# Optimization experiments

Measured on AMD Instinct MI355X. Metric: run time of the kernel, lower is better.

The kernel has to match this reference:

```python
import jax, jax.numpy as jnp
import numpy as np

TOPK = 2
NUM_EXPERTS = 8


def setup_inputs() -> dict:
    key = jax.random.key(0)
    k1, k2 = jax.random.split(key)
    T, H, E = 16384, 2048, NUM_EXPERTS
    x = jax.random.normal(k1, (T, H), dtype=jnp.float32)
    W = jax.random.normal(k2, (E, H), dtype=jnp.float32) * (1.0 / np.sqrt(H))
    return {"x": x, "W": W}


def reference(x, W):
    # gating: [T, H] @ [H, E] -> [T, E]
    logits = jnp.einsum("th,eh->te", x, W)
    # top-k expert selection (largest, sorted desc, matching torch.topk)
    top_logits, top_indices = jax.lax.top_k(logits, TOPK)
    # softmax over the k selected logits, computed in fp32 (torch: dtype=float32 then type_as)
    scores = jax.nn.softmax(top_logits.astype(jnp.float32), axis=-1).astype(logits.dtype)
    # histogram of expert assignments (torch.histc -> float counts)
    tokens_per_expert = jnp.bincount(top_indices.reshape(-1), length=NUM_EXPERTS).astype(jnp.float32)
    return scores, top_indices, tokens_per_expert
```

## Files before the change

kernel.cpp:

```cpp
#include <hip/hip_runtime.h>
#include <math.h>

#define HDIM 2048
#define NEXP 8
#define TB 4
#define WPB 4
#define TPB (TB * WPB)

__global__ void router_main(const float* __restrict__ x,
                            const float* __restrict__ W,
                            float* __restrict__ out_scores,
                            float* __restrict__ out_idx,
                            float* __restrict__ hist_global,
                            float* __restrict__ partial,
                            int T)
{
    __shared__ int cnt[NEXP];
    if (threadIdx.x < NEXP) cnt[threadIdx.x] = 0;
    __syncthreads();

    const int lane  = threadIdx.x & 63;
    const int wv    = threadIdx.x >> 6;
    const int gwave = blockIdx.x * WPB + wv;
    const int tok0  = gwave * TB;

    float acc[TB * NEXP];
#pragma unroll
    for (int i = 0; i < TB * NEXP; ++i) acc[i] = 0.f;

#pragma unroll
    for (int iter = 0; iter < HDIM / 256; ++iter) {
        const int h = iter * 256 + lane * 4;
        float4 w[NEXP];
#pragma unroll
        for (int e = 0; e < NEXP; ++e)
            w[e] = *reinterpret_cast<const float4*>(W + e * HDIM + h);
#pragma unroll
        for (int t = 0; t < TB; ++t) {
            const int tt = min(tok0 + t, T - 1);
            float4 xv = *reinterpret_cast<const float4*>(x + (size_t)tt * HDIM + h);
#pragma unroll
            for (int e = 0; e < NEXP; ++e) {
                float a = acc[t * NEXP + e];
                a = fmaf(xv.x, w[e].x, a);
                a = fmaf(xv.y, w[e].y, a);
                a = fmaf(xv.z, w[e].z, a);
                a = fmaf(xv.w, w[e].w, a);
                acc[t * NEXP + e] = a;
            }
        }
    }

#pragma unroll
    for (int j = 0; j < 32; ++j) acc[j] += __shfl_xor(acc[j], 32, 64);

#define FOLD(SM)                                                          \
    {                                                                     \
        const bool up = (lane & SM) != 0;                                 \
        _Pragma("unroll")                                                 \
        for (int j = 0; j < SM; ++j) {                                    \
            float keep = up ? acc[j + SM] : acc[j];                       \
            float send = up ? acc[j] : acc[j + SM];                       \
            acc[j] = keep + __shfl_xor(send, SM, 64);                     \
        }                                                                 \
    }
    FOLD(16) FOLD(8) FOLD(4) FOLD(2) FOLD(1)
#undef FOLD

    const int e_my   = lane & 7;
    const int t_loc  = (lane & 31) >> 3;
    const float mylg = acc[0];

    float v1 = mylg;
    int   i1 = e_my;
#pragma unroll
    for (int m = 1; m <= 4; m <<= 1) {
        float ov = __shfl_xor(v1, m, 64);
        int   oi = __shfl_xor(i1, m, 64);
        if (ov > v1 || (ov == v1 && oi < i1)) { v1 = ov; i1 = oi; }
    }
    float v2 = (e_my == i1) ? -3.402823466e+38f : mylg;
    int   i2 = e_my;
#pragma unroll
    for (int m = 1; m <= 4; m <<= 1) {
        float ov = __shfl_xor(v2, m, 64);
        int   oi = __shfl_xor(i2, m, 64);
        if (ov > v2 || (ov == v2 && oi < i2)) { v2 = ov; i2 = oi; }
    }

    const float ed = expf(v2 - v1);
    const float inv = 1.0f / (1.0f + ed);
    const float p0 = inv;
    const float p1 = ed * inv;

    const int tok = tok0 + t_loc;
    const bool leader = (lane < 32) && (e_my == 0) && (tok < T);
    if (leader) {
        out_scores[2 * tok + 0] = p0;
        out_scores[2 * tok + 1] = p1;
        out_idx[2 * tok + 0] = (float)i1;
        out_idx[2 * tok + 1] = (float)i2;
        atomicAdd(&cnt[i1], 1);
        atomicAdd(&cnt[i2], 1);
    }

    __syncthreads();
    if (threadIdx.x < NEXP) {
        if (partial)
            partial[(size_t)blockIdx.x * NEXP + threadIdx.x] = (float)cnt[threadIdx.x];
        else
            atomicAdd(&hist_global[threadIdx.x], (float)cnt[threadIdx.x]);
    }
}

__global__ void router_reduce(const float* __restrict__ partial,
                              float* __restrict__ hist, int nblocks)
{
    const int tid  = threadIdx.x;
    const int e    = tid & 7;
    const int g    = tid >> 3;
    float s = 0.f;
    for (int b = g; b < nblocks; b += 32) s += partial[(size_t)b * NEXP + e];
    s += __shfl_xor(s, 8, 64);
    s += __shfl_xor(s, 16, 64);
    s += __shfl_xor(s, 32, 64);
    __shared__ float sd[4 * NEXP];
    const int wv = tid >> 6, lane = tid & 63;
    if (lane < NEXP) sd[wv * NEXP + lane] = s;
    __syncthreads();
    if (tid < NEXP)
        hist[tid] = sd[tid] + sd[NEXP + tid] + sd[2 * NEXP + tid] + sd[3 * NEXP + tid];
}

__global__ void zero8(float* __restrict__ hist)
{
    if (threadIdx.x < NEXP) hist[threadIdx.x] = 0.f;
}

extern "C" void kernel_launch(void* const* d_in, const int* in_sizes, int n_in,
                              void* d_out, int out_size, void* d_ws, size_t ws_size,
                              hipStream_t stream)
{
    const float* x = (const float*)d_in[0];
    const float* W = (const float*)d_in[1];
    const int T = in_sizes[0] / HDIM;

    float* out        = (float*)d_out;
    float* out_scores = out;
    float* out_idx    = out + (size_t)2 * T;
    float* hist       = out + (size_t)4 * T;

    const int nblocks = (T + TPB - 1) / TPB;
    const bool use_ws = ws_size >= (size_t)nblocks * NEXP * sizeof(float);
    float* partial = use_ws ? (float*)d_ws : nullptr;

    if (!use_ws) zero8<<<1, 64, 0, stream>>>(hist);
    router_main<<<nblocks, 256, 0, stream>>>(x, W, out_scores, out_idx, hist, partial, T);
    if (use_ws) router_reduce<<<1, 256, 0, stream>>>(partial, hist, nblocks);
}
```

Measured before the change: 37.64 us.

## Process eight tokens per wave, hoist x loads, use global atomics for histogram

Each wave now handles eight tokens instead of four, so every W load is reused across twice as many tokens. The cross-lane reduction gains an extra fold step in place of the separate half-wave shuffle, and all 64 lanes hold useful results. All x loads for an iteration are issued before the W loads to raise memory-level parallelism. The partial-sum workspace and reduce kernel are replaced by a memset plus per-block float atomics on the histogram. This trades one launch for more register pressure and more global atomics.

```diff
diff --git a/kernel.cpp b/kernel.cpp
--- a/kernel.cpp
+++ b/kernel.cpp
@@ -3,26 +3,33 @@
 
 #define HDIM 2048
 #define NEXP 8
-#define TB 4
+#define TB 8
 #define WPB 4
 #define TPB (TB * WPB)
 
-__global__ void router_main(const float* __restrict__ x,
-                            const float* __restrict__ W,
-                            float* __restrict__ out_scores,
-                            float* __restrict__ out_idx,
-                            float* __restrict__ hist_global,
-                            float* __restrict__ partial,
-                            int T)
+__global__ __launch_bounds__(256) void
+router_main(const float* __restrict__ x,
+            const float* __restrict__ W,
+            float* __restrict__ out_scores,
+            float* __restrict__ out_idx,
+            float* __restrict__ hist,
+            int T)
 {
     __shared__ int cnt[NEXP];
     if (threadIdx.x < NEXP) cnt[threadIdx.x] = 0;
     __syncthreads();
 
-    const int lane  = threadIdx.x & 63;
-    const int wv    = threadIdx.x >> 6;
-    const int gwave = blockIdx.x * WPB + wv;
-    const int tok0  = gwave * TB;
+    const int lane = threadIdx.x & 63;
+    const int wv   = threadIdx.x >> 6;
+    const int tok0 = (blockIdx.x * WPB + wv) * TB;
+
+    const float* xb[TB];
+#pragma unroll
+    for (int t = 0; t < TB; ++t) {
+        int tt = tok0 + t; if (tt > T - 1) tt = T - 1;
+        xb[t] = x + (size_t)tt * HDIM + lane * 4;
+    }
+    const float* wb = W + lane * 4;
 
     float acc[TB * NEXP];
 #pragma unroll
@@ -30,29 +37,28 @@
 
 #pragma unroll
     for (int iter = 0; iter < HDIM / 256; ++iter) {
-        const int h = iter * 256 + lane * 4;
+        const int h = iter * 256;
+        float4 xv[TB];
+#pragma unroll
+        for (int t = 0; t < TB; ++t)
+            xv[t] = *reinterpret_cast<const float4*>(xb[t] + h);
         float4 w[NEXP];
 #pragma unroll
         for (int e = 0; e < NEXP; ++e)
-            w[e] = *reinterpret_cast<const float4*>(W + e * HDIM + h);
+            w[e] = *reinterpret_cast<const float4*>(wb + (size_t)e * HDIM + h);
 #pragma unroll
         for (int t = 0; t < TB; ++t) {
-            const int tt = min(tok0 + t, T - 1);
-            float4 xv = *reinterpret_cast<const float4*>(x + (size_t)tt * HDIM + h);
 #pragma unroll
             for (int e = 0; e < NEXP; ++e) {
                 float a = acc[t * NEXP + e];
-                a = fmaf(xv.x, w[e].x, a);
-                a = fmaf(xv.y, w[e].y, a);
-                a = fmaf(xv.z, w[e].z, a);
-                a = fmaf(xv.w, w[e].w, a);
+                a = fmaf(xv[t].x, w[e].x, a);
+                a = fmaf(xv[t].y, w[e].y, a);
+                a = fmaf(xv[t].z, w[e].z, a);
+                a = fmaf(xv[t].w, w[e].w, a);
                 acc[t * NEXP + e] = a;
             }
         }
     }
-
-#pragma unroll
-    for (int j = 0; j < 32; ++j) acc[j] += __shfl_xor(acc[j], 32, 64);
 
 #define FOLD(SM)                                                          \
     {                                                                     \
@@ -64,11 +70,11 @@
             acc[j] = keep + __shfl_xor(send, SM, 64);                     \
         }                                                                 \
     }
-    FOLD(16) FOLD(8) FOLD(4) FOLD(2) FOLD(1)
+    FOLD(32) FOLD(16) FOLD(8) FOLD(4) FOLD(2) FOLD(1)
 #undef FOLD
 
-    const int e_my   = lane & 7;
-    const int t_loc  = (lane & 31) >> 3;
+    const int e_my  = lane & 7;
+    const int t_loc = lane >> 3;
     const float mylg = acc[0];
 
     float v1 = mylg;
@@ -88,53 +94,20 @@
         if (ov > v2 || (ov == v2 && oi < i2)) { v2 = ov; i2 = oi; }
     }
 
-    const float ed = expf(v2 - v1);
+    const float ed  = expf(v2 - v1);
     const float inv = 1.0f / (1.0f + ed);
-    const float p0 = inv;
-    const float p1 = ed * inv;
 
     const int tok = tok0 + t_loc;
-    const bool leader = (lane < 32) && (e_my == 0) && (tok < T);
-    if (leader) {
-        out_scores[2 * tok + 0] = p0;
-        out_scores[2 * tok + 1] = p1;
-        out_idx[2 * tok + 0] = (float)i1;
-        out_idx[2 * tok + 1] = (float)i2;
+    if (e_my == 0 && tok < T) {
+        *reinterpret_cast<float2*>(out_scores + 2 * tok) = make_float2(inv, ed * inv);
+        *reinterpret_cast<float2*>(out_idx   + 2 * tok) = make_float2((float)i1, (float)i2);
         atomicAdd(&cnt[i1], 1);
         atomicAdd(&cnt[i2], 1);
     }
 
     __syncthreads();
-    if (threadIdx.x < NEXP) {
-        if (partial)
-            partial[(size_t)blockIdx.x * NEXP + threadIdx.x] = (float)cnt[threadIdx.x];
-        else
-            atomicAdd(&hist_global[threadIdx.x], (float)cnt[threadIdx.x]);
-    }
-}
-
-__global__ void router_reduce(const float* __restrict__ partial,
-                              float* __restrict__ hist, int nblocks)
-{
-    const int tid  = threadIdx.x;
-    const int e    = tid & 7;
-    const int g    = tid >> 3;
-    float s = 0.f;
-    for (int b = g; b < nblocks; b += 32) s += partial[(size_t)b * NEXP + e];
-    s += __shfl_xor(s, 8, 64);
-    s += __shfl_xor(s, 16, 64);
-    s += __shfl_xor(s, 32, 64);
-    __shared__ float sd[4 * NEXP];
-    const int wv = tid >> 6, lane = tid & 63;
-    if (lane < NEXP) sd[wv * NEXP + lane] = s;
-    __syncthreads();
-    if (tid < NEXP)
-        hist[tid] = sd[tid] + sd[NEXP + tid] + sd[2 * NEXP + tid] + sd[3 * NEXP + tid];
-}
-
-__global__ void zero8(float* __restrict__ hist)
-{
-    if (threadIdx.x < NEXP) hist[threadIdx.x] = 0.f;
+    if (threadIdx.x < NEXP)
+        atomicAdd(&hist[threadIdx.x], (float)cnt[threadIdx.x]);
 }
 
 extern "C" void kernel_launch(void* const* d_in, const int* in_sizes, int n_in,
@@ -150,11 +123,8 @@
     float* out_idx    = out + (size_t)2 * T;
     float* hist       = out + (size_t)4 * T;
 
+    hipMemsetAsync(hist, 0, NEXP * sizeof(float), stream);
+
     const int nblocks = (T + TPB - 1) / TPB;
-    const bool use_ws = ws_size >= (size_t)nblocks * NEXP * sizeof(float);
-    float* partial = use_ws ? (float*)d_ws : nullptr;
-
-    if (!use_ws) zero8<<<1, 64, 0, stream>>>(hist);
-    router_main<<<nblocks, 256, 0, stream>>>(x, W, out_scores, out_idx, hist, partial, T);
-    if (use_ws) router_reduce<<<1, 256, 0, stream>>>(partial, hist, nblocks);
+    router_main<<<nblocks, 256, 0, stream>>>(x, W, out_scores, out_idx, hist, T);
 }
```

Result: slower. 47.97 us (+27.4%).
